# Kernel tuning notes

Hardware: AMD Instinct MI355X
Metric: run time of the kernel (lower is better)

The kernel has to match this reference:

```python
import jax, jax.numpy as jnp
import numpy as np

B, K, DIM = 8192, 256, 1024


def setup_inputs() -> dict:
    key = jax.random.key(0)
    k1, k2, k3 = jax.random.split(key, 3)
    x = jax.random.normal(k1, (B, DIM), dtype=jnp.float32)
    centers = jax.random.uniform(k2, (K, DIM), dtype=jnp.float32)
    # torch init: D = 0.2 * rand + 0.9
    D = 0.2 * jax.random.uniform(k3, (K, DIM), dtype=jnp.float32) + 0.9
    return {"x": x, "centers": centers, "D": D}


def reference(x, centers, D):
    # Per-class axis-aligned (diagonal) covariance
    D_abs = jnp.abs(D) + 1e-4                      # [K, DIM]
    D_inv = 1.0 / D_abs                            # [K, DIM]
    log_det = jnp.sum(jnp.log(D_abs), axis=1)      # [K]
    det_scale_factor = -0.5 * log_det
    det_scale_safe = jnp.exp(det_scale_factor - jnp.max(det_scale_factor))  # [K]

    # dist_sq[b,k] = sum_d (x[b,d]-c[k,d])^2 * D_inv[k,d]
    # Expanded quadratic form avoids materializing the [B,K,DIM] diff tensor.
    x2 = jnp.einsum('bd,kd->bk', x * x, D_inv)             # [B, K]
    xc = jnp.einsum('bd,kd->bk', x, centers * D_inv)       # [B, K]
    c2 = jnp.sum(centers * centers * D_inv, axis=1)        # [K]
    dist_sq = x2 - 2.0 * xc + c2[None, :]                  # [B, K]

    # Gaussian path (isCauchy=False)
    expo = -0.5 * dist_sq
    expo_safe = expo - jnp.max(expo, axis=-1, keepdims=True)
    numer_safe = det_scale_safe[None, :] * jnp.exp(expo_safe)
    denom_safe = jnp.sum(numer_safe, axis=1, keepdims=True)
    resp = numer_safe / denom_safe                         # [B, K]
    return resp
```

## Files before the change

kernel.cpp:

```cpp
#include <hip/hip_runtime.h>

typedef _Float16 f16x8 __attribute__((ext_vector_type(8)));
typedef _Float16 f16x4 __attribute__((ext_vector_type(4)));
typedef float f32x4 __attribute__((ext_vector_type(4)));

#define B_N 8192
#define K_N 256
#define DIM_N 1024

__global__ __launch_bounds__(256) void prep_w(const float* __restrict__ Dm,
                                              const float* __restrict__ Cm,
                                              _Float16* __restrict__ Upk,
                                              _Float16* __restrict__ Wpk,
                                              float* __restrict__ ec) {
    const int k = blockIdx.x, t = threadIdx.x;
    const int d = t * 4;
    const float4 dv = *(const float4*)(Dm + (size_t)k * DIM_N + d);
    const float4 cv = *(const float4*)(Cm + (size_t)k * DIM_N + d);
    float dd[4] = {dv.x, dv.y, dv.z, dv.w};
    float cc[4] = {cv.x, cv.y, cv.z, cv.w};
    f16x4 uo, wo;
    float llog = 0.f, lc2 = 0.f;
#pragma unroll
    for (int i = 0; i < 4; ++i) {
        float da = fabsf(dd[i]) + 1e-4f;
        float dinv = 1.0f / da;
        llog += logf(da);
        lc2 += cc[i] * cc[i] * dinv;
        uo[i] = (_Float16)(dinv - 1.0f);
        wo[i] = (_Float16)(-2.0f * cc[i] * dinv);
    }
    const int cg = k >> 4, cl = k & 15;
    const int kc = d >> 5, g = (d >> 3) & 3, j0 = d & 7;
    const size_t off = ((size_t)(cg * 32 + kc) * 64 + g * 16 + cl) * 8 + j0;
    *(f16x4*)(Upk + off) = uo;
    *(f16x4*)(Wpk + off) = wo;
    float both = llog + lc2;
#pragma unroll
    for (int m = 1; m <= 32; m <<= 1) both += __shfl_xor(both, m, 64);
    __shared__ float sb[4];
    if ((t & 63) == 0) sb[t >> 6] = both;
    __syncthreads();
    if (t == 0) ec[k] = -0.5f * (sb[0] + sb[1] + sb[2] + sb[3]);
}

__global__ __launch_bounds__(512, 1)
void gmm_fused(const float* __restrict__ x,
               const _Float16* __restrict__ Upk,
               const _Float16* __restrict__ Wpk,
               const float* __restrict__ ecg,
               float* __restrict__ out) {
    __shared__ __align__(16) char xlds[65536];
    __shared__ float red[8][32];

    const int tid = threadIdx.x;
    const int wave = tid >> 6, lane = tid & 63;
    const int l15 = lane & 15, g4 = lane >> 4;
    const int bRow = blockIdx.x * 32;

    const int srow = tid >> 4, sd = (tid & 15) * 4;
    const float* xq = x + (size_t)(bRow + srow) * DIM_N + sd;
    int wB[4];
#pragma unroll
    for (int j = 0; j < 4; ++j) {
        const int slot = (sd >> 3) + 8 * j;
        wB[j] = srow * 512 + (((slot ^ (srow & 7)) << 4) | ((sd & 4) << 1));
    }

    const _Float16* upb = Upk + (size_t)(wave * 2) * 32 * 512 + lane * 8;
    const _Float16* wpb = Wpk + (size_t)(wave * 2) * 32 * 512 + lane * 8;

    f32x4 acc[2][2];
#pragma unroll
    for (int m = 0; m < 2; ++m)
#pragma unroll
        for (int n = 0; n < 2; ++n) { f32x4 z = {0.f, 0.f, 0.f, 0.f}; acc[m][n] = z; }

    float4 xs[2][4];
    f16x8 ub[2][2][2], wb[2][2][2];

    auto issueQ = [&](int bank, int q) {
#pragma unroll
        for (int j = 0; j < 4; ++j) xs[bank][j] = *(const float4*)(xq + q * 256 + j * 64);
    };
    auto writeQ = [&](int bank, int q) {
        char* base = xlds + q * 16384;
#pragma unroll
        for (int j = 0; j < 4; ++j) {
            const float4 v = xs[bank][j];
            f16x4 h = {(_Float16)v.x, (_Float16)v.y, (_Float16)v.z, (_Float16)v.w};
            *(f16x4*)(base + wB[j]) = h;
        }
    };
    auto issueB = [&](int bank, int c) {
#pragma unroll
        for (int n = 0; n < 2; ++n)
#pragma unroll
            for (int k2 = 0; k2 < 2; ++k2) {
                const int kc = c * 2 + k2;
                ub[bank][n][k2] = *(const f16x8*)(upb + (size_t)(n * 32 + kc) * 512);
                wb[bank][n][k2] = *(const f16x8*)(wpb + (size_t)(n * 32 + kc) * 512);
            }
    };
    auto compute = [&](int c, int bank) {
        const char* base = xlds + (c >> 2) * 16384;
        const int cl = c & 3;
        f16x8 axf[2][2], a2f[2][2];
#pragma unroll
        for (int m = 0; m < 2; ++m)
#pragma unroll
            for (int k2 = 0; k2 < 2; ++k2) {
                const int row = m * 16 + l15;
                const int slot = cl * 8 + k2 * 4 + g4;
                axf[m][k2] = *(const f16x8*)(base + row * 512 + (((slot ^ (l15 & 7)) << 4)));
                a2f[m][k2] = axf[m][k2] * axf[m][k2];
            }
        __builtin_amdgcn_s_setprio(1);
#pragma unroll
        for (int m = 0; m < 2; ++m)
#pragma unroll
            for (int n = 0; n < 2; ++n)
#pragma unroll
                for (int k2 = 0; k2 < 2; ++k2) {
                    acc[m][n] = __builtin_amdgcn_mfma_f32_16x16x32_f16(a2f[m][k2], ub[bank][n][k2], acc[m][n], 0, 0, 0);
                    acc[m][n] = __builtin_amdgcn_mfma_f32_16x16x32_f16(axf[m][k2], wb[bank][n][k2], acc[m][n], 0, 0, 0);
                }
        __builtin_amdgcn_s_setprio(0);
    };

    issueB(0, 0); issueB(1, 1);
    issueQ(0, 0); issueQ(1, 1);
    writeQ(0, 0);
    issueQ(0, 2);
    asm volatile("s_waitcnt lgkmcnt(0)" ::: "memory");
    __builtin_amdgcn_s_barrier();
    __builtin_amdgcn_sched_barrier(0);
    writeQ(1, 1);
    issueQ(1, 3);
    compute(0, 0); issueB(0, 2);
    compute(1, 1); issueB(1, 3);
    compute(2, 0); issueB(0, 4);
    compute(3, 1); issueB(1, 5);
    asm volatile("s_waitcnt lgkmcnt(0)" ::: "memory");
    __builtin_amdgcn_s_barrier();
    __builtin_amdgcn_sched_barrier(0);
    writeQ(0, 2);
    compute(4, 0); issueB(0, 6);
    compute(5, 1); issueB(1, 7);
    compute(6, 0); issueB(0, 8);
    compute(7, 1); issueB(1, 9);
    asm volatile("s_waitcnt lgkmcnt(0)" ::: "memory");
    __builtin_amdgcn_s_barrier();
    __builtin_amdgcn_sched_barrier(0);
    writeQ(1, 3);
    compute(8, 0);  issueB(0, 10);
    compute(9, 1);  issueB(1, 11);
    compute(10, 0); issueB(0, 12);
    compute(11, 1); issueB(1, 13);
    asm volatile("s_waitcnt lgkmcnt(0)" ::: "memory");
    __builtin_amdgcn_s_barrier();
    __builtin_amdgcn_sched_barrier(0);
    compute(12, 0); issueB(0, 14);
    compute(13, 1); issueB(1, 15);
    compute(14, 0);
    compute(15, 1);

    const int cls0 = wave * 32 + l15;
    const float ecv[2] = {ecg[cls0], ecg[cls0 + 16]};

    float e[2][2][4];
#pragma unroll
    for (int m = 0; m < 2; ++m)
#pragma unroll
        for (int n = 0; n < 2; ++n)
#pragma unroll
            for (int j = 0; j < 4; ++j)
                e[m][n][j] = fmaf(-0.5f, acc[m][n][j], ecv[n]);

    float mx[2][4];
#pragma unroll
    for (int m = 0; m < 2; ++m)
#pragma unroll
        for (int j = 0; j < 4; ++j) mx[m][j] = fmaxf(e[m][0][j], e[m][1][j]);
#pragma unroll
    for (int msk = 1; msk <= 8; msk <<= 1)
#pragma unroll
        for (int m = 0; m < 2; ++m)
#pragma unroll
            for (int j = 0; j < 4; ++j)
                mx[m][j] = fmaxf(mx[m][j], __shfl_xor(mx[m][j], msk, 64));
    if (l15 == 0) {
#pragma unroll
        for (int m = 0; m < 2; ++m)
#pragma unroll
            for (int j = 0; j < 4; ++j) red[wave][m * 16 + g4 * 4 + j] = mx[m][j];
    }
    __syncthreads();
    float gm[2][4];
#pragma unroll
    for (int m = 0; m < 2; ++m)
#pragma unroll
        for (int j = 0; j < 4; ++j) {
            const int r = m * 16 + g4 * 4 + j;
            float v = red[0][r];
#pragma unroll
            for (int w = 1; w < 8; ++w) v = fmaxf(v, red[w][r]);
            gm[m][j] = v;
        }
    __syncthreads();

    float p2[2][2][4], sm[2][4];
#pragma unroll
    for (int m = 0; m < 2; ++m)
#pragma unroll
        for (int j = 0; j < 4; ++j) sm[m][j] = 0.f;
#pragma unroll
    for (int m = 0; m < 2; ++m)
#pragma unroll
        for (int n = 0; n < 2; ++n)
#pragma unroll
            for (int j = 0; j < 4; ++j) {
                p2[m][n][j] = __expf(e[m][n][j] - gm[m][j]);
                sm[m][j] += p2[m][n][j];
            }
#pragma unroll
    for (int msk = 1; msk <= 8; msk <<= 1)
#pragma unroll
        for (int m = 0; m < 2; ++m)
#pragma unroll
            for (int j = 0; j < 4; ++j) sm[m][j] += __shfl_xor(sm[m][j], msk, 64);
    if (l15 == 0) {
#pragma unroll
        for (int m = 0; m < 2; ++m)
#pragma unroll
            for (int j = 0; j < 4; ++j) red[wave][m * 16 + g4 * 4 + j] = sm[m][j];
    }
    __syncthreads();
#pragma unroll
    for (int m = 0; m < 2; ++m)
#pragma unroll
        for (int j = 0; j < 4; ++j) {
            const int r = m * 16 + g4 * 4 + j;
            float t = red[0][r];
#pragma unroll
            for (int w = 1; w < 8; ++w) t += red[w][r];
            const float inv = 1.0f / t;
#pragma unroll
            for (int n = 0; n < 2; ++n)
                out[(size_t)(bRow + r) * K_N + cls0 + n * 16] = p2[m][n][j] * inv;
        }
}

extern "C" void kernel_launch(void* const* d_in, const int* in_sizes, int n_in,
                              void* d_out, int out_size, void* d_ws, size_t ws_size,
                              hipStream_t stream) {
    const float* x = (const float*)d_in[0];
    const float* cen = (const float*)d_in[1];
    const float* Dm = (const float*)d_in[2];
    float* out = (float*)d_out;

    char* ws = (char*)d_ws;
    _Float16* Upk = (_Float16*)(ws);
    _Float16* Wpk = (_Float16*)(ws + 524288);
    float* ec = (float*)(ws + 1048576);

    prep_w<<<dim3(K_N), dim3(256), 0, stream>>>(Dm, cen, Upk, Wpk, ec);
    gmm_fused<<<dim3(B_N / 32), dim3(512), 0, stream>>>(x, Upk, Wpk, ec, out);
}
```

Baseline: 29.99 us.

## Double block to 1024 threads with one 16-class tile per wave

Each block now runs 16 waves, each owning 16 classes instead of 32, so per-wave accumulators and B-operand registers are halved. X staging moves to 8-element-per-thread f16x8 LDS writes, and the softmax reductions span 16 wave partials. The aim is more latency hiding, since the former 8-wave single-block occupancy was low. The cost is twice as many threads doing redundant LDS A-fragment reads and squaring per block, plus a longer cross-wave reduction.

```diff
diff --git a/kernel.cpp b/kernel.cpp
--- a/kernel.cpp
+++ b/kernel.cpp
@@ -44,87 +44,73 @@
     if (t == 0) ec[k] = -0.5f * (sb[0] + sb[1] + sb[2] + sb[3]);
 }
 
-__global__ __launch_bounds__(512, 1)
+__global__ __launch_bounds__(1024, 1)
 void gmm_fused(const float* __restrict__ x,
                const _Float16* __restrict__ Upk,
                const _Float16* __restrict__ Wpk,
                const float* __restrict__ ecg,
                float* __restrict__ out) {
     __shared__ __align__(16) char xlds[65536];
-    __shared__ float red[8][32];
+    __shared__ float red[16][32];
 
     const int tid = threadIdx.x;
     const int wave = tid >> 6, lane = tid & 63;
     const int l15 = lane & 15, g4 = lane >> 4;
     const int bRow = blockIdx.x * 32;
 
-    const int srow = tid >> 4, sd = (tid & 15) * 4;
+    const int srow = tid >> 5, sd = (tid & 31) * 8;
     const float* xq = x + (size_t)(bRow + srow) * DIM_N + sd;
-    int wB[4];
-#pragma unroll
-    for (int j = 0; j < 4; ++j) {
-        const int slot = (sd >> 3) + 8 * j;
-        wB[j] = srow * 512 + (((slot ^ (srow & 7)) << 4) | ((sd & 4) << 1));
-    }
-
-    const _Float16* upb = Upk + (size_t)(wave * 2) * 32 * 512 + lane * 8;
-    const _Float16* wpb = Wpk + (size_t)(wave * 2) * 32 * 512 + lane * 8;
-
-    f32x4 acc[2][2];
-#pragma unroll
-    for (int m = 0; m < 2; ++m)
-#pragma unroll
-        for (int n = 0; n < 2; ++n) { f32x4 z = {0.f, 0.f, 0.f, 0.f}; acc[m][n] = z; }
-
-    float4 xs[2][4];
-    f16x8 ub[2][2][2], wb[2][2][2];
+    const int wByte = srow * 512 + ((((sd >> 3) ^ (srow & 7)) << 4));
+
+    const _Float16* upb = Upk + (size_t)wave * 32 * 512 + lane * 8;
+    const _Float16* wpb = Wpk + (size_t)wave * 32 * 512 + lane * 8;
+
+    f32x4 acc[2];
+#pragma unroll
+    for (int m = 0; m < 2; ++m) { f32x4 z = {0.f, 0.f, 0.f, 0.f}; acc[m] = z; }
+
+    float4 xs[2][2];
+    f16x8 ub[2][2], wb[2][2];
 
     auto issueQ = [&](int bank, int q) {
-#pragma unroll
-        for (int j = 0; j < 4; ++j) xs[bank][j] = *(const float4*)(xq + q * 256 + j * 64);
+        xs[bank][0] = *(const float4*)(xq + q * 256);
+        xs[bank][1] = *(const float4*)(xq + q * 256 + 4);
     };
     auto writeQ = [&](int bank, int q) {
-        char* base = xlds + q * 16384;
-#pragma unroll
-        for (int j = 0; j < 4; ++j) {
-            const float4 v = xs[bank][j];
-            f16x4 h = {(_Float16)v.x, (_Float16)v.y, (_Float16)v.z, (_Float16)v.w};
-            *(f16x4*)(base + wB[j]) = h;
-        }
+        const float4 a = xs[bank][0], b = xs[bank][1];
+        f16x8 h = {(_Float16)a.x, (_Float16)a.y, (_Float16)a.z, (_Float16)a.w,
+                   (_Float16)b.x, (_Float16)b.y, (_Float16)b.z, (_Float16)b.w};
+        *(f16x8*)(xlds + q * 16384 + wByte) = h;
     };
     auto issueB = [&](int bank, int c) {
 #pragma unroll
-        for (int n = 0; n < 2; ++n)
-#pragma unroll
-            for (int k2 = 0; k2 < 2; ++k2) {
-                const int kc = c * 2 + k2;
-                ub[bank][n][k2] = *(const f16x8*)(upb + (size_t)(n * 32 + kc) * 512);
-                wb[bank][n][k2] = *(const f16x8*)(wpb + (size_t)(n * 32 + kc) * 512);
-            }
+        for (int k2 = 0; k2 < 2; ++k2) {
+            const int kc = c * 2 + k2;
+            ub[bank][k2] = *(const f16x8*)(upb + (size_t)kc * 512);
+            wb[bank][k2] = *(const f16x8*)(wpb + (size_t)kc * 512);
+        }
     };
     auto compute = [&](int c, int bank) {
         const char* base = xlds + (c >> 2) * 16384;
         const int cl = c & 3;
-        f16x8 axf[2][2], a2f[2][2];
+        f16x8 axf[2][2];
 #pragma unroll
         for (int m = 0; m < 2; ++m)
 #pragma unroll
             for (int k2 = 0; k2 < 2; ++k2) {
                 const int row = m * 16 + l15;
                 const int slot = cl * 8 + k2 * 4 + g4;
-                axf[m][k2] = *(const f16x8*)(base + row * 512 + (((slot ^ (l15 & 7)) << 4)));
-                a2f[m][k2] = axf[m][k2] * axf[m][k2];
+                axf[m][k2] = *(const f16x8*)(base + row * 512 + ((slot ^ (l15 & 7)) << 4));
             }
         __builtin_amdgcn_s_setprio(1);
 #pragma unroll
         for (int m = 0; m < 2; ++m)
 #pragma unroll
-            for (int n = 0; n < 2; ++n)
-#pragma unroll
-                for (int k2 = 0; k2 < 2; ++k2) {
-                    acc[m][n] = __builtin_amdgcn_mfma_f32_16x16x32_f16(a2f[m][k2], ub[bank][n][k2], acc[m][n], 0, 0, 0);
-                    acc[m][n] = __builtin_amdgcn_mfma_f32_16x16x32_f16(axf[m][k2], wb[bank][n][k2], acc[m][n], 0, 0, 0);
-                }
+            for (int k2 = 0; k2 < 2; ++k2) {
+                const f16x8 a2 = axf[m][k2] * axf[m][k2];
+                acc[m] = __builtin_amdgcn_mfma_f32_16x16x32_f16(a2, ub[bank][k2], acc[m], 0, 0, 0);
+                acc[m] = __builtin_amdgcn_mfma_f32_16x16x32_f16(axf[m][k2], wb[bank][k2], acc[m], 0, 0, 0);
+            }
         __builtin_amdgcn_s_setprio(0);
     };
 
@@ -165,23 +151,21 @@
     compute(14, 0);
     compute(15, 1);
 
-    const int cls0 = wave * 32 + l15;
-    const float ecv[2] = {ecg[cls0], ecg[cls0 + 16]};
-
-    float e[2][2][4];
-#pragma unroll
-    for (int m = 0; m < 2; ++m)
-#pragma unroll
-        for (int n = 0; n < 2; ++n)
-#pragma unroll
-            for (int j = 0; j < 4; ++j)
-                e[m][n][j] = fmaf(-0.5f, acc[m][n][j], ecv[n]);
+    const int cls0 = wave * 16 + l15;
+    const float ecv = ecg[cls0];
+
+    float e[2][4];
+#pragma unroll
+    for (int m = 0; m < 2; ++m)
+#pragma unroll
+        for (int j = 0; j < 4; ++j)
+            e[m][j] = fmaf(-0.5f, acc[m][j], ecv);
 
     float mx[2][4];
 #pragma unroll
     for (int m = 0; m < 2; ++m)
 #pragma unroll
-        for (int j = 0; j < 4; ++j) mx[m][j] = fmaxf(e[m][0][j], e[m][1][j]);
+        for (int j = 0; j < 4; ++j) mx[m][j] = e[m][j];
 #pragma unroll
     for (int msk = 1; msk <= 8; msk <<= 1)
 #pragma unroll
@@ -204,25 +188,19 @@
             const int r = m * 16 + g4 * 4 + j;
             float v = red[0][r];
 #pragma unroll
-            for (int w = 1; w < 8; ++w) v = fmaxf(v, red[w][r]);
+            for (int w = 1; w < 16; ++w) v = fmaxf(v, red[w][r]);
             gm[m][j] = v;
         }
     __syncthreads();
 
-    float p2[2][2][4], sm[2][4];
-#pragma unroll
-    for (int m = 0; m < 2; ++m)
-#pragma unroll
-        for (int j = 0; j < 4; ++j) sm[m][j] = 0.f;
-#pragma unroll
-    for (int m = 0; m < 2; ++m)
-#pragma unroll
-        for (int n = 0; n < 2; ++n)
-#pragma unroll
-            for (int j = 0; j < 4; ++j) {
-                p2[m][n][j] = __expf(e[m][n][j] - gm[m][j]);
-                sm[m][j] += p2[m][n][j];
-            }
+    float p2[2][4], sm[2][4];
+#pragma unroll
+    for (int m = 0; m < 2; ++m)
+#pragma unroll
+        for (int j = 0; j < 4; ++j) {
+            p2[m][j] = __expf(e[m][j] - gm[m][j]);
+            sm[m][j] = p2[m][j];
+        }
 #pragma unroll
     for (int msk = 1; msk <= 8; msk <<= 1)
 #pragma unroll
@@ -243,11 +221,8 @@
             const int r = m * 16 + g4 * 4 + j;
             float t = red[0][r];
 #pragma unroll
-            for (int w = 1; w < 8; ++w) t += red[w][r];
-            const float inv = 1.0f / t;
-#pragma unroll
-            for (int n = 0; n < 2; ++n)
-                out[(size_t)(bRow + r) * K_N + cls0 + n * 16] = p2[m][n][j] * inv;
+            for (int w = 1; w < 16; ++w) t += red[w][r];
+            out[(size_t)(bRow + r) * K_N + cls0] = p2[m][j] / t;
         }
 }
 
@@ -265,5 +240,5 @@
     float* ec = (float*)(ws + 1048576);
 
     prep_w<<<dim3(K_N), dim3(256), 0, stream>>>(Dm, cen, Upk, Wpk, ec);
-    gmm_fused<<<dim3(B_N / 32), dim3(512), 0, stream>>>(x, Upk, Wpk, ec, out);
+    gmm_fused<<<dim3(B_N / 32), dim3(1024), 0, stream>>>(x, Upk, Wpk, ec, out);
 }
```

After: 32.76 us. 9.2% more time.

## Store x tile in MFMA fragment order and triple-buffer weight fragments

Applied to the files above, without the earlier changes.

Changes the shared-memory layout of the fp16 x tile so each lane's MFMA A-fragment is stored contiguously. Fragment reads become simple lane*16 offsets, and each thread writes two 16-byte vectors instead of four 8-byte swizzled writes. Weight/U fragment prefetch moves from two to three register banks, so global loads are issued further ahead of use. It also interleaves the squaring with the MFMAs and drops the s_setprio hints, which raises register pressure under launch_bounds(512,1).

```diff
diff --git a/kernel.cpp b/kernel.cpp
--- a/kernel.cpp
+++ b/kernel.cpp
@@ -58,14 +58,13 @@
     const int l15 = lane & 15, g4 = lane >> 4;
     const int bRow = blockIdx.x * 32;
 
-    const int srow = tid >> 4, sd = (tid & 15) * 4;
-    const float* xq = x + (size_t)(bRow + srow) * DIM_N + sd;
-    int wB[4];
-#pragma unroll
-    for (int j = 0; j < 4; ++j) {
-        const int slot = (sd >> 3) + 8 * j;
-        wB[j] = srow * 512 + (((slot ^ (srow & 7)) << 4) | ((sd & 4) << 1));
-    }
+    const int srow = tid >> 4, sdq = tid & 15;
+    const float* xq = x + (size_t)(bRow + srow) * DIM_N + sdq * 16;
+    const int smq = srow >> 4, r15 = srow & 15;
+    const int scl = sdq >> 2;
+    const int dc0 = (sdq & 3) * 16;
+    const int sk2 = dc0 >> 5, sgb = (dc0 >> 3) & 3;
+    const int wOff = scl * 4096 + (smq * 2 + sk2) * 1024 + (r15 + sgb * 16) * 16;
 
     const _Float16* upb = Upk + (size_t)(wave * 2) * 32 * 512 + lane * 8;
     const _Float16* wpb = Wpk + (size_t)(wave * 2) * 32 * 512 + lane * 8;
@@ -77,20 +76,20 @@
         for (int n = 0; n < 2; ++n) { f32x4 z = {0.f, 0.f, 0.f, 0.f}; acc[m][n] = z; }
 
     float4 xs[2][4];
-    f16x8 ub[2][2][2], wb[2][2][2];
+    f16x8 ub[3][2][2], wb[3][2][2];
 
     auto issueQ = [&](int bank, int q) {
 #pragma unroll
-        for (int j = 0; j < 4; ++j) xs[bank][j] = *(const float4*)(xq + q * 256 + j * 64);
+        for (int j = 0; j < 4; ++j) xs[bank][j] = *(const float4*)(xq + q * 256 + j * 4);
     };
     auto writeQ = [&](int bank, int q) {
-        char* base = xlds + q * 16384;
-#pragma unroll
-        for (int j = 0; j < 4; ++j) {
-            const float4 v = xs[bank][j];
-            f16x4 h = {(_Float16)v.x, (_Float16)v.y, (_Float16)v.z, (_Float16)v.w};
-            *(f16x4*)(base + wB[j]) = h;
-        }
+        const float4 a = xs[bank][0], b = xs[bank][1], c = xs[bank][2], d = xs[bank][3];
+        f16x8 h0 = {(_Float16)a.x, (_Float16)a.y, (_Float16)a.z, (_Float16)a.w,
+                    (_Float16)b.x, (_Float16)b.y, (_Float16)b.z, (_Float16)b.w};
+        f16x8 h1 = {(_Float16)c.x, (_Float16)c.y, (_Float16)c.z, (_Float16)c.w,
+                    (_Float16)d.x, (_Float16)d.y, (_Float16)d.z, (_Float16)d.w};
+        *(f16x8*)(xlds + q * 16384 + wOff) = h0;
+        *(f16x8*)(xlds + q * 16384 + wOff + 256) = h1;
     };
     auto issueB = [&](int bank, int c) {
 #pragma unroll
@@ -103,32 +102,27 @@
             }
     };
     auto compute = [&](int c, int bank) {
-        const char* base = xlds + (c >> 2) * 16384;
-        const int cl = c & 3;
-        f16x8 axf[2][2], a2f[2][2];
+        const char* base = xlds + c * 4096;
+        f16x8 axf[2][2];
+#pragma unroll
+        for (int m = 0; m < 2; ++m)
+#pragma unroll
+            for (int k2 = 0; k2 < 2; ++k2)
+                axf[m][k2] = *(const f16x8*)(base + (m * 2 + k2) * 1024 + lane * 16);
 #pragma unroll
         for (int m = 0; m < 2; ++m)
 #pragma unroll
             for (int k2 = 0; k2 < 2; ++k2) {
-                const int row = m * 16 + l15;
-                const int slot = cl * 8 + k2 * 4 + g4;
-                axf[m][k2] = *(const f16x8*)(base + row * 512 + (((slot ^ (l15 & 7)) << 4)));
-                a2f[m][k2] = axf[m][k2] * axf[m][k2];
-            }
-        __builtin_amdgcn_s_setprio(1);
-#pragma unroll
-        for (int m = 0; m < 2; ++m)
-#pragma unroll
-            for (int n = 0; n < 2; ++n)
-#pragma unroll
-                for (int k2 = 0; k2 < 2; ++k2) {
-                    acc[m][n] = __builtin_amdgcn_mfma_f32_16x16x32_f16(a2f[m][k2], ub[bank][n][k2], acc[m][n], 0, 0, 0);
+                const f16x8 a2 = axf[m][k2] * axf[m][k2];
+#pragma unroll
+                for (int n = 0; n < 2; ++n) {
+                    acc[m][n] = __builtin_amdgcn_mfma_f32_16x16x32_f16(a2, ub[bank][n][k2], acc[m][n], 0, 0, 0);
                     acc[m][n] = __builtin_amdgcn_mfma_f32_16x16x32_f16(axf[m][k2], wb[bank][n][k2], acc[m][n], 0, 0, 0);
                 }
-        __builtin_amdgcn_s_setprio(0);
-    };
-
-    issueB(0, 0); issueB(1, 1);
+            }
+    };
+
+    issueB(0, 0); issueB(1, 1); issueB(2, 2);
     issueQ(0, 0); issueQ(1, 1);
     writeQ(0, 0);
     issueQ(0, 2);
@@ -137,33 +131,33 @@
     __builtin_amdgcn_sched_barrier(0);
     writeQ(1, 1);
     issueQ(1, 3);
-    compute(0, 0); issueB(0, 2);
-    compute(1, 1); issueB(1, 3);
-    compute(2, 0); issueB(0, 4);
-    compute(3, 1); issueB(1, 5);
+    compute(0, 0);  issueB(0, 3);
+    compute(1, 1);  issueB(1, 4);
+    compute(2, 2);  issueB(2, 5);
+    compute(3, 0);  issueB(0, 6);
     asm volatile("s_waitcnt lgkmcnt(0)" ::: "memory");
     __builtin_amdgcn_s_barrier();
     __builtin_amdgcn_sched_barrier(0);
     writeQ(0, 2);
-    compute(4, 0); issueB(0, 6);
-    compute(5, 1); issueB(1, 7);
-    compute(6, 0); issueB(0, 8);
-    compute(7, 1); issueB(1, 9);
+    compute(4, 1);  issueB(1, 7);
+    compute(5, 2);  issueB(2, 8);
+    compute(6, 0);  issueB(0, 9);
+    compute(7, 1);  issueB(1, 10);
     asm volatile("s_waitcnt lgkmcnt(0)" ::: "memory");
     __builtin_amdgcn_s_barrier();
     __builtin_amdgcn_sched_barrier(0);
     writeQ(1, 3);
-    compute(8, 0);  issueB(0, 10);
-    compute(9, 1);  issueB(1, 11);
-    compute(10, 0); issueB(0, 12);
-    compute(11, 1); issueB(1, 13);
-    asm volatile("s_waitcnt lgkmcnt(0)" ::: "memory");
-    __builtin_amdgcn_s_barrier();
-    __builtin_amdgcn_sched_barrier(0);
-    compute(12, 0); issueB(0, 14);
-    compute(13, 1); issueB(1, 15);
-    compute(14, 0);
-    compute(15, 1);
+    compute(8, 2);   issueB(2, 11);
+    compute(9, 0);   issueB(0, 12);
+    compute(10, 1);  issueB(1, 13);
+    compute(11, 2);  issueB(2, 14);
+    asm volatile("s_waitcnt lgkmcnt(0)" ::: "memory");
+    __builtin_amdgcn_s_barrier();
+    __builtin_amdgcn_sched_barrier(0);
+    compute(12, 0);  issueB(0, 15);
+    compute(13, 1);
+    compute(14, 2);
+    compute(15, 0);
 
     const int cls0 = wave * 32 + l15;
     const float ecv[2] = {ecg[cls0], ecg[cls0 + 16]};
@@ -209,11 +203,11 @@
         }
     __syncthreads();
 
-    float p2[2][2][4], sm[2][4];
-#pragma unroll
-    for (int m = 0; m < 2; ++m)
-#pragma unroll
-        for (int j = 0; j < 4; ++j) sm[m][j] = 0.f;
+    float p2[2][2][4], sfs[2][4];
+#pragma unroll
+    for (int m = 0; m < 2; ++m)
+#pragma unroll
+        for (int j = 0; j < 4; ++j) sfs[m][j] = 0.f;
 #pragma unroll
     for (int m = 0; m < 2; ++m)
 #pragma unroll
@@ -221,19 +215,19 @@
 #pragma unroll
             for (int j = 0; j < 4; ++j) {
                 p2[m][n][j] = __expf(e[m][n][j] - gm[m][j]);
-                sm[m][j] += p2[m][n][j];
+                sfs[m][j] += p2[m][n][j];
             }
 #pragma unroll
     for (int msk = 1; msk <= 8; msk <<= 1)
 #pragma unroll
         for (int m = 0; m < 2; ++m)
 #pragma unroll
-            for (int j = 0; j < 4; ++j) sm[m][j] += __shfl_xor(sm[m][j], msk, 64);
+            for (int j = 0; j < 4; ++j) sfs[m][j] += __shfl_xor(sfs[m][j], msk, 64);
     if (l15 == 0) {
 #pragma unroll
         for (int m = 0; m < 2; ++m)
 #pragma unroll
-            for (int j = 0; j < 4; ++j) red[wave][m * 16 + g4 * 4 + j] = sm[m][j];
+            for (int j = 0; j < 4; ++j) red[wave][m * 16 + g4 * 4 + j] = sfs[m][j];
     }
     __syncthreads();
 #pragma unroll
```

New measurement: 30.89 us. 3.0% more time.
